# Performance work log

Measured on AMD Instinct MI355X. Metric: run time of the kernel, lower is better.

Reference implementation:

```python
import jax, jax.numpy as jnp
import numpy as np

WEIGHT = 0.1
SELF_WEIGHT = 1.0
OTHER_WEIGHT = 1.0

def setup_inputs() -> dict:
    key = jax.random.key(0)
    k1, k2 = jax.random.split(key)
    B, D = 8192, 128
    output = jax.random.normal(k1, (B, D), dtype=jnp.float32)
    target = jax.random.normal(k2, (B, D), dtype=jnp.float32)
    return {"output": output, "target": target}

def reference(output, target):
    # Pairwise Euclidean distances d[i, n] = ||output[i] - target[n]||_2
    # no [B, B, D] intermediate).
    B = output.shape[0]
    xx = jnp.sum(output * output, axis=-1)          # [B]
    yy = jnp.sum(target * target, axis=-1)          # [B]
    d2 = xx[:, None] + yy[None, :] - 2.0 * (output @ target.T)  # [B, B]
    d = jnp.sqrt(jnp.maximum(d2, 0.0))
    diag_sum = jnp.trace(d)                          # sum of self distances
    total_sum = jnp.sum(d)
    other_sum = total_sum - diag_sum
    loss = (-diag_sum * SELF_WEIGHT + other_sum * OTHER_WEIGHT) / B * WEIGHT
    return loss
```

## Files before the change

### kernel.cpp

```cpp
#include <hip/hip_runtime.h>
#include <stdint.h>

typedef float f32x16 __attribute__((ext_vector_type(16)));

#define BDIM 8192

__device__ __forceinline__ void gload16(const void* g, void* l) {
    __builtin_amdgcn_global_load_lds(
        (const __attribute__((address_space(1))) uint32_t*)g,
        (__attribute__((address_space(3))) uint32_t*)l,
        16, 0, 0);
}

__global__ __launch_bounds__(256) void prep_kernel(const float* __restrict__ out_f,
                                                   const float* __restrict__ tgt_f,
                                                   uint8_t* __restrict__ ak,
                                                   float* __restrict__ xxyy) {
    const float* src = blockIdx.y ? tgt_f : out_f;
    uint8_t* dst = ak + (size_t)blockIdx.y * (1u << 20);
    float* nrm = xxyy + (size_t)blockIdx.y * BDIM;

    const int tid = threadIdx.x;
    const int lane = tid & 63;
    const int w = tid >> 6;
    const int j = lane & 15;
    const int r = blockIdx.x * 16 + w * 4 + (lane >> 4);

    const float4* s4 = (const float4*)(src + (size_t)r * 128 + j * 8);
    float4 a = s4[0], b = s4[1];

    uint32_t w0 = __builtin_amdgcn_cvt_pk_fp8_f32(a.x, a.y, 0, false);
    w0 = __builtin_amdgcn_cvt_pk_fp8_f32(a.z, a.w, w0, true);
    uint32_t w1 = __builtin_amdgcn_cvt_pk_fp8_f32(b.x, b.y, 0, false);
    w1 = __builtin_amdgcn_cvt_pk_fp8_f32(b.z, b.w, w1, true);
    *(uint2*)(dst + j * 65536 + r * 8) = make_uint2(w0, w1);

    float sq = a.x*a.x + a.y*a.y + a.z*a.z + a.w*a.w
             + b.x*b.x + b.y*b.y + b.z*b.z + b.w*b.w;
    sq += __shfl_xor(sq, 1); sq += __shfl_xor(sq, 2);
    sq += __shfl_xor(sq, 4); sq += __shfl_xor(sq, 8);
    if (j == 0) nrm[r] = sq;
}

__global__ __launch_bounds__(256, 4) void dist_kernel(const uint8_t* __restrict__ Ak,
                                                      const uint8_t* __restrict__ Bk,
                                                      const float* __restrict__ xxg,
                                                      const float* __restrict__ yyg,
                                                      float* __restrict__ partials) {
    __shared__ uint8_t Al[16384];
    __shared__ uint8_t Bl[16384];
    __shared__ float xxl[128];
    __shared__ float yyl[128];
    __shared__ float wsum[4];

    const int tid = threadIdx.x;
    const int lane = tid & 63;
    const int wid = tid >> 6;
    const int wr = wid >> 1, wc = wid & 1;
    const int bx = blockIdx.x, by = blockIdx.y;

    if (tid < 128) xxl[tid] = xxg[bx * 128 + tid];
    else           yyl[tid - 128] = yyg[by * 128 + (tid - 128)];

    {
        const uint8_t* ga = Ak + wid * 65536 + bx * 1024 + lane * 16;
        const uint8_t* gb = Bk + wid * 65536 + by * 1024 + lane * 16;
        uint8_t* la = Al + tid * 16;
        uint8_t* lb = Bl + tid * 16;
        #pragma unroll
        for (int i = 0; i < 4; ++i) {
            gload16(ga + i * 262144, la + i * 4096);
            gload16(gb + i * 262144, lb + i * 4096);
        }
    }
    __syncthreads();

    const int lm = lane & 31;
    const int fh = lane >> 5;
    const uint8_t* abase = Al + fh * 1024 + (wr * 64 + lm) * 8;
    const uint8_t* bbase = Bl + fh * 1024 + (wc * 64 + lm) * 8;

    f32x16 acc[2][2] = {};
    #pragma unroll
    for (int s = 0; s < 8; ++s) {
        long a0 = *(const long*)(abase + s * 2048);
        long a1 = *(const long*)(abase + s * 2048 + 256);
        long b0 = *(const long*)(bbase + s * 2048);
        long b1 = *(const long*)(bbase + s * 2048 + 256);
        acc[0][0] = __builtin_amdgcn_mfma_f32_32x32x16_fp8_fp8(a0, b0, acc[0][0], 0, 0, 0);
        acc[0][1] = __builtin_amdgcn_mfma_f32_32x32x16_fp8_fp8(a0, b1, acc[0][1], 0, 0, 0);
        acc[1][0] = __builtin_amdgcn_mfma_f32_32x32x16_fp8_fp8(a1, b0, acc[1][0], 0, 0, 0);
        acc[1][1] = __builtin_amdgcn_mfma_f32_32x32x16_fp8_fp8(a1, b1, acc[1][1], 0, 0, 0);
    }

    float s0 = 0.0f, s1 = 0.0f;
    #pragma unroll
    for (int tr = 0; tr < 2; ++tr) {
        float xv[16];
        #pragma unroll
        for (int r = 0; r < 16; ++r) {
            int ml = wr * 64 + tr * 32 + (r & 3) + 8 * (r >> 2) + 4 * fh;
            xv[r] = xxl[ml];
        }
        #pragma unroll
        for (int tc = 0; tc < 2; ++tc) {
            float yv = yyl[wc * 64 + tc * 32 + lm];
            #pragma unroll
            for (int r = 0; r < 16; ++r) {
                float d2 = fmaf(-2.0f, acc[tr][tc][r], xv[r] + yv);
                float d = __builtin_amdgcn_sqrtf(fmaxf(d2, 0.0f));
                if (r & 1) s1 += d; else s0 += d;
            }
        }
    }
    float s = s0 + s1;

    if (bx == by && wr == wc) {
        #pragma unroll
        for (int t = 0; t < 2; ++t) {
            #pragma unroll
            for (int r = 0; r < 16; ++r) {
                int row = (r & 3) + 8 * (r >> 2) + 4 * fh;
                if (row == lm) {
                    int idx = wr * 64 + t * 32 + row;
                    float d2 = fmaf(-2.0f, acc[t][t][r], xxl[idx] + yyl[idx]);
                    s -= 2.0f * __builtin_amdgcn_sqrtf(fmaxf(d2, 0.0f));
                }
            }
        }
    }

    #pragma unroll
    for (int off = 32; off > 0; off >>= 1) s += __shfl_down(s, off);
    if (lane == 0) wsum[wid] = s;
    __syncthreads();
    if (tid == 0) partials[by * 64 + bx] = wsum[0] + wsum[1] + wsum[2] + wsum[3];
}

__global__ __launch_bounds__(256) void reduce_kernel(const float* __restrict__ partials,
                                                     float* __restrict__ out) {
    __shared__ float wsum[4];
    float s = 0.0f;
    for (int i = threadIdx.x; i < 4096; i += 256) s += partials[i];
    #pragma unroll
    for (int off = 32; off > 0; off >>= 1) s += __shfl_down(s, off);
    int lane = threadIdx.x & 63, wid = threadIdx.x >> 6;
    if (lane == 0) wsum[wid] = s;
    __syncthreads();
    if (threadIdx.x == 0)
        out[0] = (wsum[0] + wsum[1] + wsum[2] + wsum[3]) * (0.1f / 8192.0f);
}

extern "C" void kernel_launch(void* const* d_in, const int* in_sizes, int n_in,
                              void* d_out, int out_size, void* d_ws, size_t ws_size,
                              hipStream_t stream) {
    const float* output = (const float*)d_in[0];
    const float* target = (const float*)d_in[1];

    uint8_t* ws = (uint8_t*)d_ws;
    uint8_t* ak      = ws;
    float*   xxyy    = (float*)(ws + 2u * 1024u * 1024u);
    float*   partial = (float*)(ws + 2u * 1024u * 1024u + 64u * 1024u);

    prep_kernel<<<dim3(512, 2), 256, 0, stream>>>(output, target, ak, xxyy);
    dist_kernel<<<dim3(64, 64), 256, 0, stream>>>(ak, ak + (1u << 20),
                                                  xxyy, xxyy + BDIM, partial);
    reduce_kernel<<<1, 256, 0, stream>>>(partial, (float*)d_out);
}
```

Measured before the change: 84.16 us.

## Load fp8 operands directly from global into registers, dropping LDS staging

The prep kernel now writes fp8 data row-major, 128 bytes per row with a permuted K ordering, instead of K-chunk-major. The distance kernel drops the LDS tiles and the global_load_lds staging and reads 16-byte vectors straight from global memory into MFMA operand registers, relying on cache reuse across blocks. This removes LDS traffic and reduces shared memory use, which may help occupancy. It exposes global memory latency with no staging or prefetch, and the K permutation must match between A and B for the dot product to stay correct.

```diff
diff --git a/kernel.cpp b/kernel.cpp
--- a/kernel.cpp
+++ b/kernel.cpp
@@ -2,15 +2,9 @@
 #include <stdint.h>
 
 typedef float f32x16 __attribute__((ext_vector_type(16)));
+typedef long long2v __attribute__((ext_vector_type(2)));
 
 #define BDIM 8192
-
-__device__ __forceinline__ void gload16(const void* g, void* l) {
-    __builtin_amdgcn_global_load_lds(
-        (const __attribute__((address_space(1))) uint32_t*)g,
-        (__attribute__((address_space(3))) uint32_t*)l,
-        16, 0, 0);
-}
 
 __global__ __launch_bounds__(256) void prep_kernel(const float* __restrict__ out_f,
                                                    const float* __restrict__ tgt_f,
@@ -23,23 +17,23 @@
     const int tid = threadIdx.x;
     const int lane = tid & 63;
     const int w = tid >> 6;
-    const int j = lane & 15;
+    const int jg = lane & 15;
     const int r = blockIdx.x * 16 + w * 4 + (lane >> 4);
 
-    const float4* s4 = (const float4*)(src + (size_t)r * 128 + j * 8);
+    const float4* s4 = (const float4*)(src + (size_t)r * 128 + jg * 8);
     float4 a = s4[0], b = s4[1];
 
     uint32_t w0 = __builtin_amdgcn_cvt_pk_fp8_f32(a.x, a.y, 0, false);
     w0 = __builtin_amdgcn_cvt_pk_fp8_f32(a.z, a.w, w0, true);
     uint32_t w1 = __builtin_amdgcn_cvt_pk_fp8_f32(b.x, b.y, 0, false);
     w1 = __builtin_amdgcn_cvt_pk_fp8_f32(b.z, b.w, w1, true);
-    *(uint2*)(dst + j * 65536 + r * 8) = make_uint2(w0, w1);
+    *(uint2*)(dst + r * 128 + (jg & 1) * 64 + (jg >> 1) * 8) = make_uint2(w0, w1);
 
     float sq = a.x*a.x + a.y*a.y + a.z*a.z + a.w*a.w
              + b.x*b.x + b.y*b.y + b.z*b.z + b.w*b.w;
     sq += __shfl_xor(sq, 1); sq += __shfl_xor(sq, 2);
     sq += __shfl_xor(sq, 4); sq += __shfl_xor(sq, 8);
-    if (j == 0) nrm[r] = sq;
+    if (jg == 0) nrm[r] = sq;
 }
 
 __global__ __launch_bounds__(256, 4) void dist_kernel(const uint8_t* __restrict__ Ak,
@@ -47,8 +41,6 @@
                                                       const float* __restrict__ xxg,
                                                       const float* __restrict__ yyg,
                                                       float* __restrict__ partials) {
-    __shared__ uint8_t Al[16384];
-    __shared__ uint8_t Bl[16384];
     __shared__ float xxl[128];
     __shared__ float yyl[128];
     __shared__ float wsum[4];
@@ -61,36 +53,37 @@
 
     if (tid < 128) xxl[tid] = xxg[bx * 128 + tid];
     else           yyl[tid - 128] = yyg[by * 128 + (tid - 128)];
-
-    {
-        const uint8_t* ga = Ak + wid * 65536 + bx * 1024 + lane * 16;
-        const uint8_t* gb = Bk + wid * 65536 + by * 1024 + lane * 16;
-        uint8_t* la = Al + tid * 16;
-        uint8_t* lb = Bl + tid * 16;
-        #pragma unroll
-        for (int i = 0; i < 4; ++i) {
-            gload16(ga + i * 262144, la + i * 4096);
-            gload16(gb + i * 262144, lb + i * 4096);
-        }
-    }
     __syncthreads();
 
     const int lm = lane & 31;
     const int fh = lane >> 5;
-    const uint8_t* abase = Al + fh * 1024 + (wr * 64 + lm) * 8;
-    const uint8_t* bbase = Bl + fh * 1024 + (wc * 64 + lm) * 8;
+    const uint8_t* arow = Ak + ((size_t)(bx * 128 + wr * 64 + lm) << 7) + (fh << 6);
+    const uint8_t* brow = Bk + ((size_t)(by * 128 + wc * 64 + lm) << 7) + (fh << 6);
 
     f32x16 acc[2][2] = {};
     #pragma unroll
-    for (int s = 0; s < 8; ++s) {
-        long a0 = *(const long*)(abase + s * 2048);
-        long a1 = *(const long*)(abase + s * 2048 + 256);
-        long b0 = *(const long*)(bbase + s * 2048);
-        long b1 = *(const long*)(bbase + s * 2048 + 256);
-        acc[0][0] = __builtin_amdgcn_mfma_f32_32x32x16_fp8_fp8(a0, b0, acc[0][0], 0, 0, 0);
-        acc[0][1] = __builtin_amdgcn_mfma_f32_32x32x16_fp8_fp8(a0, b1, acc[0][1], 0, 0, 0);
-        acc[1][0] = __builtin_amdgcn_mfma_f32_32x32x16_fp8_fp8(a1, b0, acc[1][0], 0, 0, 0);
-        acc[1][1] = __builtin_amdgcn_mfma_f32_32x32x16_fp8_fp8(a1, b1, acc[1][1], 0, 0, 0);
+    for (int h = 0; h < 2; ++h) {
+        long2v av[2][2], bv[2][2];
+        #pragma unroll
+        for (int t = 0; t < 2; ++t) {
+            #pragma unroll
+            for (int u = 0; u < 2; ++u) {
+                av[t][u] = *(const long2v*)(arow + t * 4096 + h * 32 + u * 16);
+                bv[t][u] = *(const long2v*)(brow + t * 4096 + h * 32 + u * 16);
+            }
+        }
+        #pragma unroll
+        for (int u = 0; u < 2; ++u) {
+            #pragma unroll
+            for (int p = 0; p < 2; ++p) {
+                long a0 = av[0][u][p], a1 = av[1][u][p];
+                long b0 = bv[0][u][p], b1 = bv[1][u][p];
+                acc[0][0] = __builtin_amdgcn_mfma_f32_32x32x16_fp8_fp8(a0, b0, acc[0][0], 0, 0, 0);
+                acc[0][1] = __builtin_amdgcn_mfma_f32_32x32x16_fp8_fp8(a0, b1, acc[0][1], 0, 0, 0);
+                acc[1][0] = __builtin_amdgcn_mfma_f32_32x32x16_fp8_fp8(a1, b0, acc[1][0], 0, 0, 0);
+                acc[1][1] = __builtin_amdgcn_mfma_f32_32x32x16_fp8_fp8(a1, b1, acc[1][1], 0, 0, 0);
+            }
+        }
     }
 
     float s0 = 0.0f, s1 = 0.0f;
```

After: 98.86 us. 1.17x slower.

## Loop each block over four B tiles reusing the A tile, with wider LDS reads

Applied to the files above, without the earlier changes.

Each dist_kernel block now keeps its A tile resident and iterates over four consecutive B column tiles, reloading only B into LDS between iterations. The grid shrinks from 4096 to 1024 blocks, and the reduce kernel reads 1024 partials. The prep kernel repacks the fp8 layout so each lane reads 16 bytes per LDS load, feeding two MFMAs. fmax is replaced by fabs before sqrt and the accumulation is split across four partial sums. The goal is to cut redundant A loads and per-block launch/sync overhead; the cost is serialized B reloads behind syncthreads and fewer blocks for latency hiding.

```diff
diff --git a/kernel.cpp b/kernel.cpp
--- a/kernel.cpp
+++ b/kernel.cpp
@@ -2,6 +2,7 @@
 #include <stdint.h>
 
 typedef float f32x16 __attribute__((ext_vector_type(16)));
+typedef long long2v __attribute__((ext_vector_type(2)));
 
 #define BDIM 8192
 
@@ -23,23 +24,26 @@
     const int tid = threadIdx.x;
     const int lane = tid & 63;
     const int w = tid >> 6;
-    const int j = lane & 15;
+    const int jg = lane & 15;
     const int r = blockIdx.x * 16 + w * 4 + (lane >> 4);
 
-    const float4* s4 = (const float4*)(src + (size_t)r * 128 + j * 8);
+    const float4* s4 = (const float4*)(src + (size_t)r * 128 + jg * 8);
     float4 a = s4[0], b = s4[1];
 
     uint32_t w0 = __builtin_amdgcn_cvt_pk_fp8_f32(a.x, a.y, 0, false);
     w0 = __builtin_amdgcn_cvt_pk_fp8_f32(a.z, a.w, w0, true);
     uint32_t w1 = __builtin_amdgcn_cvt_pk_fp8_f32(b.x, b.y, 0, false);
     w1 = __builtin_amdgcn_cvt_pk_fp8_f32(b.z, b.w, w1, true);
-    *(uint2*)(dst + j * 65536 + r * 8) = make_uint2(w0, w1);
+
+    const int Q   = (jg & 1) * 4 + (jg >> 2);
+    const int odd = (jg >> 1) & 1;
+    *(uint2*)(dst + Q * 131072 + r * 16 + odd * 8) = make_uint2(w0, w1);
 
     float sq = a.x*a.x + a.y*a.y + a.z*a.z + a.w*a.w
              + b.x*b.x + b.y*b.y + b.z*b.z + b.w*b.w;
     sq += __shfl_xor(sq, 1); sq += __shfl_xor(sq, 2);
     sq += __shfl_xor(sq, 4); sq += __shfl_xor(sq, 8);
-    if (j == 0) nrm[r] = sq;
+    if (jg == 0) nrm[r] = sq;
 }
 
 __global__ __launch_bounds__(256, 4) void dist_kernel(const uint8_t* __restrict__ Ak,
@@ -50,98 +54,118 @@
     __shared__ uint8_t Al[16384];
     __shared__ uint8_t Bl[16384];
     __shared__ float xxl[128];
-    __shared__ float yyl[128];
+    __shared__ float yyl[512];
     __shared__ float wsum[4];
 
     const int tid = threadIdx.x;
     const int lane = tid & 63;
     const int wid = tid >> 6;
     const int wr = wid >> 1, wc = wid & 1;
-    const int bx = blockIdx.x, by = blockIdx.y;
+    const int bx = blockIdx.x & 63;
+    const int byg = blockIdx.x >> 6;
 
+    const int rq = tid >> 7;
+    const int rr = tid & 127;
+    const uint8_t* ga = Ak + rq * 131072 + bx * 2048 + rr * 16;
+    const uint8_t* gb0 = Bk + rq * 131072 + (size_t)byg * 4 * 2048 + rr * 16;
+    uint8_t* la = Al + tid * 16;
+    uint8_t* lb = Bl + tid * 16;
+
+    #pragma unroll
+    for (int i = 0; i < 4; ++i) {
+        gload16(ga + i * 262144, la + i * 4096);
+        gload16(gb0 + i * 262144, lb + i * 4096);
+    }
     if (tid < 128) xxl[tid] = xxg[bx * 128 + tid];
-    else           yyl[tid - 128] = yyg[by * 128 + (tid - 128)];
-
-    {
-        const uint8_t* ga = Ak + wid * 65536 + bx * 1024 + lane * 16;
-        const uint8_t* gb = Bk + wid * 65536 + by * 1024 + lane * 16;
-        uint8_t* la = Al + tid * 16;
-        uint8_t* lb = Bl + tid * 16;
-        #pragma unroll
-        for (int i = 0; i < 4; ++i) {
-            gload16(ga + i * 262144, la + i * 4096);
-            gload16(gb + i * 262144, lb + i * 4096);
-        }
-    }
+    yyl[tid]       = yyg[byg * 512 + tid];
+    yyl[tid + 256] = yyg[byg * 512 + 256 + tid];
     __syncthreads();
 
     const int lm = lane & 31;
     const int fh = lane >> 5;
-    const uint8_t* abase = Al + fh * 1024 + (wr * 64 + lm) * 8;
-    const uint8_t* bbase = Bl + fh * 1024 + (wc * 64 + lm) * 8;
+    const uint8_t* abase = Al + fh * 8192 + (wr * 64 + lm) * 16;
+    const uint8_t* bbase = Bl + fh * 8192 + (wc * 64 + lm) * 16;
 
-    f32x16 acc[2][2] = {};
+    float s0 = 0.0f, s1 = 0.0f, s2 = 0.0f, s3 = 0.0f;
+
     #pragma unroll
-    for (int s = 0; s < 8; ++s) {
-        long a0 = *(const long*)(abase + s * 2048);
-        long a1 = *(const long*)(abase + s * 2048 + 256);
-        long b0 = *(const long*)(bbase + s * 2048);
-        long b1 = *(const long*)(bbase + s * 2048 + 256);
-        acc[0][0] = __builtin_amdgcn_mfma_f32_32x32x16_fp8_fp8(a0, b0, acc[0][0], 0, 0, 0);
-        acc[0][1] = __builtin_amdgcn_mfma_f32_32x32x16_fp8_fp8(a0, b1, acc[0][1], 0, 0, 0);
-        acc[1][0] = __builtin_amdgcn_mfma_f32_32x32x16_fp8_fp8(a1, b0, acc[1][0], 0, 0, 0);
-        acc[1][1] = __builtin_amdgcn_mfma_f32_32x32x16_fp8_fp8(a1, b1, acc[1][1], 0, 0, 0);
-    }
+    for (int j = 0; j < 4; ++j) {
+        if (j) __syncthreads();
 
-    float s0 = 0.0f, s1 = 0.0f;
-    #pragma unroll
-    for (int tr = 0; tr < 2; ++tr) {
-        float xv[16];
+        f32x16 acc[2][2] = {};
         #pragma unroll
-        for (int r = 0; r < 16; ++r) {
-            int ml = wr * 64 + tr * 32 + (r & 3) + 8 * (r >> 2) + 4 * fh;
-            xv[r] = xxl[ml];
+        for (int p = 0; p < 4; ++p) {
+            long2v a0 = *(const long2v*)(abase + p * 2048);
+            long2v a1 = *(const long2v*)(abase + p * 2048 + 512);
+            long2v b0 = *(const long2v*)(bbase + p * 2048);
+            long2v b1 = *(const long2v*)(bbase + p * 2048 + 512);
+            #pragma unroll
+            for (int e = 0; e < 2; ++e) {
+                acc[0][0] = __builtin_amdgcn_mfma_f32_32x32x16_fp8_fp8(a0[e], b0[e], acc[0][0], 0, 0, 0);
+                acc[0][1] = __builtin_amdgcn_mfma_f32_32x32x16_fp8_fp8(a0[e], b1[e], acc[0][1], 0, 0, 0);
+                acc[1][0] = __builtin_amdgcn_mfma_f32_32x32x16_fp8_fp8(a1[e], b0[e], acc[1][0], 0, 0, 0);
+                acc[1][1] = __builtin_amdgcn_mfma_f32_32x32x16_fp8_fp8(a1[e], b1[e], acc[1][1], 0, 0, 0);
+            }
         }
+        __syncthreads();
+
+        if (j < 3) {
+            const uint8_t* gb = gb0 + (j + 1) * 2048;
+            #pragma unroll
+            for (int i = 0; i < 4; ++i) gload16(gb + i * 262144, lb + i * 4096);
+        }
+
         #pragma unroll
-        for (int tc = 0; tc < 2; ++tc) {
-            float yv = yyl[wc * 64 + tc * 32 + lm];
+        for (int tr = 0; tr < 2; ++tr) {
+            float xv[16];
             #pragma unroll
             for (int r = 0; r < 16; ++r) {
-                float d2 = fmaf(-2.0f, acc[tr][tc][r], xv[r] + yv);
-                float d = __builtin_amdgcn_sqrtf(fmaxf(d2, 0.0f));
-                if (r & 1) s1 += d; else s0 += d;
+                int ml = wr * 64 + tr * 32 + (r & 3) + 8 * (r >> 2) + 4 * fh;
+                xv[r] = xxl[ml];
+            }
+            #pragma unroll
+            for (int tc = 0; tc < 2; ++tc) {
+                float yv = yyl[j * 128 + wc * 64 + tc * 32 + lm];
+                #pragma unroll
+                for (int r = 0; r < 16; ++r) {
+                    float d2 = fmaf(-2.0f, acc[tr][tc][r], xv[r] + yv);
+                    float d = __builtin_amdgcn_sqrtf(__builtin_fabsf(d2));
+                    if (r & 3) { if ((r & 3) == 1) s1 += d; else if ((r & 3) == 2) s2 += d; else s3 += d; }
+                    else s0 += d;
+                }
             }
         }
-    }
-    float s = s0 + s1;
 
-    if (bx == by && wr == wc) {
-        #pragma unroll
-        for (int t = 0; t < 2; ++t) {
+        if (bx == byg * 4 + j && wr == wc) {
             #pragma unroll
-            for (int r = 0; r < 16; ++r) {
-                int row = (r & 3) + 8 * (r >> 2) + 4 * fh;
-                if (row == lm) {
-                    int idx = wr * 64 + t * 32 + row;
-                    float d2 = fmaf(-2.0f, acc[t][t][r], xxl[idx] + yyl[idx]);
-                    s -= 2.0f * __builtin_amdgcn_sqrtf(fmaxf(d2, 0.0f));
+            for (int t = 0; t < 2; ++t) {
+                #pragma unroll
+                for (int r = 0; r < 16; ++r) {
+                    int row = (r & 3) + 8 * (r >> 2) + 4 * fh;
+                    if (row == lm) {
+                        int idx = wr * 64 + t * 32 + row;
+                        float d2 = fmaf(-2.0f, acc[t][t][r], xxl[idx] + yyl[j * 128 + idx]);
+                        s0 -= 2.0f * __builtin_amdgcn_sqrtf(__builtin_fabsf(d2));
+                    }
                 }
             }
         }
     }
 
+    float s = (s0 + s1) + (s2 + s3);
     #pragma unroll
     for (int off = 32; off > 0; off >>= 1) s += __shfl_down(s, off);
     if (lane == 0) wsum[wid] = s;
     __syncthreads();
-    if (tid == 0) partials[by * 64 + bx] = wsum[0] + wsum[1] + wsum[2] + wsum[3];
+    if (tid == 0) partials[blockIdx.x] = wsum[0] + wsum[1] + wsum[2] + wsum[3];
 }
 
 __global__ __launch_bounds__(256) void reduce_kernel(const float* __restrict__ partials,
                                                      float* __restrict__ out) {
     __shared__ float wsum[4];
     float s = 0.0f;
-    for (int i = threadIdx.x; i < 4096; i += 256) s += partials[i];
+    #pragma unroll
+    for (int i = 0; i < 4; ++i) s += partials[threadIdx.x + i * 256];
     #pragma unroll
     for (int off = 32; off > 0; off >>= 1) s += __shfl_down(s, off);
     int lane = threadIdx.x & 63, wid = threadIdx.x >> 6;
@@ -163,7 +187,7 @@
     float*   partial = (float*)(ws + 2u * 1024u * 1024u + 64u * 1024u);
 
     prep_kernel<<<dim3(512, 2), 256, 0, stream>>>(output, target, ak, xxyy);
-    dist_kernel<<<dim3(64, 64), 256, 0, stream>>>(ak, ak + (1u << 20),
-                                                  xxyy, xxyy + BDIM, partial);
+    dist_kernel<<<dim3(1024), 256, 0, stream>>>(ak, ak + (1u << 20),
+                                                xxyy, xxyy + BDIM, partial);
     reduce_kernel<<<1, 256, 0, stream>>>(partial, (float*)d_out);
 }
```

Result: slower. 134.8 us (+60.2%).

## Halve dist kernel tile width to 128x64 and double grid for occupancy

Applied to the files above, without the earlier changes.

The distance kernel now computes 128x64 output tiles instead of 128x128, launching twice as many blocks. Each wave holds two accumulators instead of four, LDS use drops, and launch bounds ask for five blocks per CU. The aim is more resident waves and better load balance across CUs, at the cost of reloading the A tile twice as often and lower MFMA reuse per LDS load. It also replaces fmax(d2,0) with fabs before sqrt and fully unrolls the reduce loop.

```diff
diff --git a/kernel.cpp b/kernel.cpp
--- a/kernel.cpp
+++ b/kernel.cpp
@@ -23,109 +23,97 @@
     const int tid = threadIdx.x;
     const int lane = tid & 63;
     const int w = tid >> 6;
-    const int j = lane & 15;
+    const int jg = lane & 15;
     const int r = blockIdx.x * 16 + w * 4 + (lane >> 4);
 
-    const float4* s4 = (const float4*)(src + (size_t)r * 128 + j * 8);
+    const float4* s4 = (const float4*)(src + (size_t)r * 128 + jg * 8);
     float4 a = s4[0], b = s4[1];
 
     uint32_t w0 = __builtin_amdgcn_cvt_pk_fp8_f32(a.x, a.y, 0, false);
     w0 = __builtin_amdgcn_cvt_pk_fp8_f32(a.z, a.w, w0, true);
     uint32_t w1 = __builtin_amdgcn_cvt_pk_fp8_f32(b.x, b.y, 0, false);
     w1 = __builtin_amdgcn_cvt_pk_fp8_f32(b.z, b.w, w1, true);
-    *(uint2*)(dst + j * 65536 + r * 8) = make_uint2(w0, w1);
+    *(uint2*)(dst + jg * 65536 + r * 8) = make_uint2(w0, w1);
 
     float sq = a.x*a.x + a.y*a.y + a.z*a.z + a.w*a.w
              + b.x*b.x + b.y*b.y + b.z*b.z + b.w*b.w;
     sq += __shfl_xor(sq, 1); sq += __shfl_xor(sq, 2);
     sq += __shfl_xor(sq, 4); sq += __shfl_xor(sq, 8);
-    if (j == 0) nrm[r] = sq;
+    if (jg == 0) nrm[r] = sq;
 }
 
-__global__ __launch_bounds__(256, 4) void dist_kernel(const uint8_t* __restrict__ Ak,
+__global__ __launch_bounds__(256, 5) void dist_kernel(const uint8_t* __restrict__ Ak,
                                                       const uint8_t* __restrict__ Bk,
                                                       const float* __restrict__ xxg,
                                                       const float* __restrict__ yyg,
                                                       float* __restrict__ partials) {
     __shared__ uint8_t Al[16384];
-    __shared__ uint8_t Bl[16384];
+    __shared__ uint8_t Bl[8192];
     __shared__ float xxl[128];
-    __shared__ float yyl[128];
+    __shared__ float yyl[64];
     __shared__ float wsum[4];
 
     const int tid = threadIdx.x;
     const int lane = tid & 63;
     const int wid = tid >> 6;
     const int wr = wid >> 1, wc = wid & 1;
-    const int bx = blockIdx.x, by = blockIdx.y;
-
-    if (tid < 128) xxl[tid] = xxg[bx * 128 + tid];
-    else           yyl[tid - 128] = yyg[by * 128 + (tid - 128)];
+    const int bx = blockIdx.x;
+    const int by2 = blockIdx.y;
 
     {
-        const uint8_t* ga = Ak + wid * 65536 + bx * 1024 + lane * 16;
-        const uint8_t* gb = Bk + wid * 65536 + by * 1024 + lane * 16;
-        uint8_t* la = Al + tid * 16;
-        uint8_t* lb = Bl + tid * 16;
+        const uint8_t* ga = Ak + (tid >> 6) * 65536 + bx * 1024 + (tid & 63) * 16;
+        uint8_t* la = (uint8_t*)Al + tid * 16;
         #pragma unroll
-        for (int i = 0; i < 4; ++i) {
-            gload16(ga + i * 262144, la + i * 4096);
-            gload16(gb + i * 262144, lb + i * 4096);
-        }
+        for (int i = 0; i < 4; ++i) gload16(ga + i * 262144, la + i * 4096);
     }
+    {
+        const uint8_t* gb = Bk + (tid >> 5) * 65536 + by2 * 512 + (tid & 31) * 16;
+        uint8_t* lb = (uint8_t*)Bl + tid * 16;
+        #pragma unroll
+        for (int i = 0; i < 2; ++i) gload16(gb + i * 524288, lb + i * 4096);
+    }
+    if (tid < 128) xxl[tid] = xxg[bx * 128 + tid];
+    else if (tid < 192) yyl[tid - 128] = yyg[by2 * 64 + (tid - 128)];
     __syncthreads();
 
     const int lm = lane & 31;
     const int fh = lane >> 5;
-    const uint8_t* abase = Al + fh * 1024 + (wr * 64 + lm) * 8;
-    const uint8_t* bbase = Bl + fh * 1024 + (wc * 64 + lm) * 8;
+    const uint8_t* abase = Al + fh * 1024 + wr * 512 + lm * 8;
+    const uint8_t* bbase = Bl + fh * 512 + wc * 256 + lm * 8;
 
-    f32x16 acc[2][2] = {};
+    f32x16 acc0 = {}, acc1 = {};
     #pragma unroll
     for (int s = 0; s < 8; ++s) {
         long a0 = *(const long*)(abase + s * 2048);
         long a1 = *(const long*)(abase + s * 2048 + 256);
-        long b0 = *(const long*)(bbase + s * 2048);
-        long b1 = *(const long*)(bbase + s * 2048 + 256);
-        acc[0][0] = __builtin_amdgcn_mfma_f32_32x32x16_fp8_fp8(a0, b0, acc[0][0], 0, 0, 0);
-        acc[0][1] = __builtin_amdgcn_mfma_f32_32x32x16_fp8_fp8(a0, b1, acc[0][1], 0, 0, 0);
-        acc[1][0] = __builtin_amdgcn_mfma_f32_32x32x16_fp8_fp8(a1, b0, acc[1][0], 0, 0, 0);
-        acc[1][1] = __builtin_amdgcn_mfma_f32_32x32x16_fp8_fp8(a1, b1, acc[1][1], 0, 0, 0);
+        long b0 = *(const long*)(bbase + s * 1024);
+        acc0 = __builtin_amdgcn_mfma_f32_32x32x16_fp8_fp8(a0, b0, acc0, 0, 0, 0);
+        acc1 = __builtin_amdgcn_mfma_f32_32x32x16_fp8_fp8(a1, b0, acc1, 0, 0, 0);
     }
 
+    float yv = yyl[wc * 32 + lm];
     float s0 = 0.0f, s1 = 0.0f;
     #pragma unroll
-    for (int tr = 0; tr < 2; ++tr) {
-        float xv[16];
+    for (int t = 0; t < 2; ++t) {
+        const f32x16& av = t ? acc1 : acc0;
         #pragma unroll
         for (int r = 0; r < 16; ++r) {
-            int ml = wr * 64 + tr * 32 + (r & 3) + 8 * (r >> 2) + 4 * fh;
-            xv[r] = xxl[ml];
-        }
-        #pragma unroll
-        for (int tc = 0; tc < 2; ++tc) {
-            float yv = yyl[wc * 64 + tc * 32 + lm];
-            #pragma unroll
-            for (int r = 0; r < 16; ++r) {
-                float d2 = fmaf(-2.0f, acc[tr][tc][r], xv[r] + yv);
-                float d = __builtin_amdgcn_sqrtf(fmaxf(d2, 0.0f));
-                if (r & 1) s1 += d; else s0 += d;
-            }
+            int ml = wr * 64 + t * 32 + (r & 3) + 8 * (r >> 2) + 4 * fh;
+            float d2 = fmaf(-2.0f, av[r], xxl[ml] + yv);
+            float d = __builtin_amdgcn_sqrtf(__builtin_fabsf(d2));
+            if (r & 1) s1 += d; else s0 += d;
         }
     }
     float s = s0 + s1;
 
-    if (bx == by && wr == wc) {
+    if ((by2 >> 1) == bx && wr == (by2 & 1)) {
+        const f32x16& av = wc ? acc1 : acc0;
         #pragma unroll
-        for (int t = 0; t < 2; ++t) {
-            #pragma unroll
-            for (int r = 0; r < 16; ++r) {
-                int row = (r & 3) + 8 * (r >> 2) + 4 * fh;
-                if (row == lm) {
-                    int idx = wr * 64 + t * 32 + row;
-                    float d2 = fmaf(-2.0f, acc[t][t][r], xxl[idx] + yyl[idx]);
-                    s -= 2.0f * __builtin_amdgcn_sqrtf(fmaxf(d2, 0.0f));
-                }
+        for (int r = 0; r < 16; ++r) {
+            int rp = (r & 3) + 8 * (r >> 2) + 4 * fh;
+            if (rp == lm) {
+                float d2 = fmaf(-2.0f, av[r], xxl[wr * 64 + wc * 32 + rp] + yyl[wc * 32 + rp]);
+                s -= 2.0f * __builtin_amdgcn_sqrtf(__builtin_fabsf(d2));
             }
         }
     }
@@ -134,14 +122,15 @@
     for (int off = 32; off > 0; off >>= 1) s += __shfl_down(s, off);
     if (lane == 0) wsum[wid] = s;
     __syncthreads();
-    if (tid == 0) partials[by * 64 + bx] = wsum[0] + wsum[1] + wsum[2] + wsum[3];
+    if (tid == 0) partials[by2 * 64 + bx] = wsum[0] + wsum[1] + wsum[2] + wsum[3];
 }
 
 __global__ __launch_bounds__(256) void reduce_kernel(const float* __restrict__ partials,
                                                      float* __restrict__ out) {
     __shared__ float wsum[4];
     float s = 0.0f;
-    for (int i = threadIdx.x; i < 4096; i += 256) s += partials[i];
+    #pragma unroll
+    for (int i = 0; i < 32; ++i) s += partials[threadIdx.x + i * 256];
     #pragma unroll
     for (int off = 32; off > 0; off >>= 1) s += __shfl_down(s, off);
     int lane = threadIdx.x & 63, wid = threadIdx.x >> 6;
@@ -163,7 +152,7 @@
     float*   partial = (float*)(ws + 2u * 1024u * 1024u + 64u * 1024u);
 
     prep_kernel<<<dim3(512, 2), 256, 0, stream>>>(output, target, ak, xxyy);
-    dist_kernel<<<dim3(64, 64), 256, 0, stream>>>(ak, ak + (1u << 20),
-                                                  xxyy, xxyy + BDIM, partial);
+    dist_kernel<<<dim3(64, 128), 256, 0, stream>>>(ak, ak + (1u << 20),
+                                                   xxyy, xxyy + BDIM, partial);
     reduce_kernel<<<1, 256, 0, stream>>>(partial, (float*)d_out);
 }
```

New measurement: 81.97 us. 1.03x faster.
